# Performance work log

Measured on AMD Instinct MI355X. Metric: run time of the kernel, lower is better.

## Reference

```python
import jax, jax.numpy as jnp
import numpy as np

VOCAB = 32000      # embedding vocab
EMBED = 300        # nn.Embedding embedding_dim
HID = 256          # sequence_size // 2 per direction (sequence_size=512)
N_COLS = 4096      # number of columns (split-delimited segments)
SEG_LEN = 8        # 7 description words + 1 SPLIT token per column
SPLIT_IDX = 0
T = N_COLS * SEG_LEN


def setup_inputs() -> dict:
    key = jax.random.key(0)
    ks = jax.random.split(key, 10)
    # tokens in [1, VOCAB), with SPLIT_IDX at the end of every SEG_LEN block
    seq = jax.random.randint(ks[0], (T,), 1, VOCAB)
    seq = seq.at[SEG_LEN - 1::SEG_LEN].set(SPLIT_IDX)
    s = 1.0 / np.sqrt(HID)  # torch LSTM default init range

    def u(k, shape):
        return jax.random.uniform(k, shape, jnp.float32, -s, s)

    return {
        "emb_table": jax.random.normal(ks[1], (VOCAB, EMBED), jnp.float32),
        "w_ih_f": u(ks[2], (4 * HID, EMBED)),
        "w_hh_f": u(ks[3], (4 * HID, HID)),
        "b_ih_f": u(ks[4], (4 * HID,)),
        "b_hh_f": u(ks[5], (4 * HID,)),
        "w_ih_b": u(ks[6], (4 * HID, EMBED)),
        "w_hh_b": u(ks[7], (4 * HID, HID)),
        "b_ih_b": u(ks[8], (4 * HID,)),
        "b_hh_b": u(ks[9], (4 * HID,)),
        "seq_s": seq,
    }


def _run_dir(xg, mask, w_hh, reverse):
    """Masked LSTM over time. xg: [L, N, 4H] precomputed input gates (+bias),
    mask: [L, N] validity per original time index. Returns final hidden [N, H]."""
    if reverse:
        xg = xg[::-1]
        mask = mask[::-1]
    N = xg.shape[1]

    def step(carry, inp):
        h, c = carry
        g, m = inp
        gates = g + h @ w_hh.T                       # [N, 4H]
        i, f, gg, o = jnp.split(gates, 4, axis=-1)   # torch gate order i,f,g,o
        c_new = jax.nn.sigmoid(f) * c + jax.nn.sigmoid(i) * jnp.tanh(gg)
        h_new = jax.nn.sigmoid(o) * jnp.tanh(c_new)
        m = m[:, None]
        return (jnp.where(m, h_new, h), jnp.where(m, c_new, c)), None

    init = (jnp.zeros((N, HID), xg.dtype), jnp.zeros((N, HID), xg.dtype))
    (h, _), _ = jax.lax.scan(step, init, (xg, mask))
    return h


def reference(emb_table, w_ih_f, w_hh_f, b_ih_f, b_hh_f,
              w_ih_b, w_hh_b, b_ih_b, b_hh_b, seq_s):
    col = jnp.arange(N_COLS)
    # torch code: ends = nonzero(split); begins = roll(ends,1); begins[0] = 0
    # => segment i>0 starts AT the previous split token (len SEG_LEN);
    #    segment 0 is [0, SEG_LEN-1) (len SEG_LEN-1).
    begins = jnp.where(col == 0, 0, col * SEG_LEN - 1)
    lengths = jnp.where(col == 0, SEG_LEN - 1, SEG_LEN)
    idx = jnp.clip(begins[:, None] + jnp.arange(SEG_LEN)[None, :], 0, T - 1)  # [N, L]
    mask = jnp.arange(SEG_LEN)[None, :] < lengths[:, None]                    # [N, L]

    segs = emb_table[seq_s][idx]        # [N, L, E] embedded ragged segments
    x = segs.transpose(1, 0, 2)          # [L, N, E]
    m = mask.T                           # [L, N]

    xg_f = jnp.einsum('lne,ge->lng', x, w_ih_f) + b_ih_f + b_hh_f
    xg_b = jnp.einsum('lne,ge->lng', x, w_ih_b) + b_ih_b + b_hh_b
    h_f = _run_dir(xg_f, m, w_hh_f, reverse=False)   # forward final hidden
    h_b = _run_dir(xg_b, m, w_hh_b, reverse=True)    # backward final hidden (t=0)
    # torch final_hidden.view(-1) per column == concat(fwd, bwd)
    return jnp.concatenate([h_f, h_b], axis=-1)      # [N_COLS, 2*HID]
```

## Files before the change

### kernel.cpp

```cpp
#include <hip/hip_runtime.h>

typedef unsigned int uint;
typedef unsigned short ushort;
typedef __attribute__((ext_vector_type(8))) short short8;
typedef __attribute__((ext_vector_type(4))) float f32x4;
typedef __attribute__((ext_vector_type(4))) uint uint4w;

#define T_LEN 32768
#define EMB 300
#define HID 256
#define NCOLS 4096

__device__ __forceinline__ ushort f2bf(float f) {
  uint u = __float_as_uint(f);
  return (ushort)((u + 0x7fffu + ((u >> 16) & 1u)) >> 16);
}
__device__ __forceinline__ float bf2f(ushort u) {
  return __uint_as_float(((uint)u) << 16);
}
__device__ __forceinline__ float sigm(float x) { return 1.f / (1.f + __expf(-x)); }
__device__ __forceinline__ float tanh_(float x) { return 2.f / (1.f + __expf(-2.f * x)) - 1.f; }

__device__ __forceinline__ void gload_lds16(const void* g, void* l) {
  __builtin_amdgcn_global_load_lds((const __attribute__((address_space(1))) void*)g,
                                   (__attribute__((address_space(3))) void*)l, 16, 0, 0);
}

__global__ void prep_kernel(const float* __restrict__ emb,
                            const float* __restrict__ wihf, const float* __restrict__ whhf,
                            const float* __restrict__ bihf, const float* __restrict__ bhhf,
                            const float* __restrict__ wihb, const float* __restrict__ whhb,
                            const float* __restrict__ bihb, const float* __restrict__ bhhb,
                            const int* __restrict__ seq,
                            ushort* __restrict__ X, ushort* __restrict__ Wih,
                            ushort* __restrict__ Whh, float* __restrict__ bias) {
  const int NX = T_LEN * 40;
  const int NWIH = 2048 * 40;
  const int NWHH = 2048 * 32;
  const int NB = 2048;
  const int total = NX + NWIH + NWHH + NB;
  for (int t = blockIdx.x * blockDim.x + threadIdx.x; t < total; t += gridDim.x * blockDim.x) {
    if (t < NX) {
      int r = t / 40, k8 = t % 40, k = k8 * 8;
      int col = r >> 3, j = r & 7;
      int tok = (col == 0) ? j : (col * 8 - 1 + j);
      const float* src = emb + (long)seq[tok] * EMB + k;
      alignas(16) ushort tmp[8];
#pragma unroll
      for (int i = 0; i < 8; ++i) tmp[i] = (k + i < EMB) ? f2bf(src[i]) : (ushort)0;
      *(uint4w*)(X + (long)r * 320 + k) = *(const uint4w*)tmp;
    } else if (t < NX + NWIH) {
      int t2 = t - NX;
      int n = t2 / 40, k8 = t2 % 40, k = k8 * 8;
      const float* src = ((n < 1024) ? wihf : wihb) + (long)(n & 1023) * EMB + k;
      alignas(16) ushort tmp[8];
#pragma unroll
      for (int i = 0; i < 8; ++i) tmp[i] = (k + i < EMB) ? f2bf(src[i]) : (ushort)0;
      *(uint4w*)(Wih + (long)n * 320 + k) = *(const uint4w*)tmp;
    } else if (t < NX + NWIH + NWHH) {
      int t3 = t - NX - NWIH;
      int n = t3 / 32, k8 = t3 % 32, k = k8 * 8;
      const float* src = ((n < 1024) ? whhf : whhb) + (long)(n & 1023) * HID + k;
      alignas(16) ushort tmp[8];
#pragma unroll
      for (int i = 0; i < 8; ++i) tmp[i] = f2bf(src[i]);
      *(uint4w*)(Whh + (long)n * 256 + k) = *(const uint4w*)tmp;
    } else {
      int n = t - NX - NWIH - NWHH;
      bias[n] = (n < 1024) ? (bihf[n] + bhhf[n]) : (bihb[n - 1024] + bhhb[n - 1024]);
    }
  }
}

__global__ void gemm_xg_kernel(const ushort* __restrict__ X, const ushort* __restrict__ Wih,
                               const float* __restrict__ bias, ushort* __restrict__ xg) {
  __shared__ ushort a_lds[2][128 * 32];
  const int tid = threadIdx.x;
  const int lane = tid & 63, w = tid >> 6;
  const int wr = w >> 1, wc = w & 1;
  const int qrow = lane >> 4, ln = lane & 15;
  const int m0 = blockIdx.x * 128, n0 = blockIdx.y * 128;

  auto stage = [&](int buf, int kt) {
#pragma unroll
    for (int q = 0; q < 2; ++q) {
      int byteoff = w * 2048 + q * 1024 + lane * 16;
      int row = byteoff >> 6, koff = byteoff & 63;
      const char* src = (const char*)X + (long)(m0 + row) * 640 + kt * 64 + koff;
      void* dst = (char*)&a_lds[buf][0] + w * 2048 + q * 1024;
      gload_lds16(src, dst);
    }
  };

  const ushort* wb = Wih + (long)(n0 + wc * 64 + ln) * 320 + qrow * 8;
  auto loadB = [&](short8 (&dst)[4], int kt) {
#pragma unroll
    for (int nt = 0; nt < 4; ++nt)
      dst[nt] = *(const short8*)(wb + nt * 16 * 320 + kt * 32);
  };

  const f32x4 fzero = {0.f, 0.f, 0.f, 0.f};
  f32x4 acc[4][4];
#pragma unroll
  for (int i = 0; i < 4; ++i)
#pragma unroll
    for (int jj = 0; jj < 4; ++jj) acc[i][jj] = fzero;

  auto gemmK = [&](short8 (&b)[4], int buf) {
    short8 a[4];
#pragma unroll
    for (int rt = 0; rt < 4; ++rt)
      a[rt] = *(const short8*)&a_lds[buf][(wr * 64 + rt * 16 + ln) * 32 + qrow * 8];
#pragma unroll
    for (int rt = 0; rt < 4; ++rt)
#pragma unroll
      for (int nt = 0; nt < 4; ++nt)
        acc[rt][nt] = __builtin_amdgcn_mfma_f32_16x16x32_bf16(a[rt], b[nt], acc[rt][nt], 0, 0, 0);
  };

  short8 bA[4], bB[4];
  stage(0, 0);
  loadB(bA, 0);
#pragma unroll 1
  for (int kt2 = 0; kt2 < 5; ++kt2) {
    const int kt = kt2 * 2;
    __syncthreads();
    loadB(bB, kt + 1);
    __builtin_amdgcn_sched_barrier(0);
    if (kt < 9) stage(1, kt + 1);
    __builtin_amdgcn_sched_barrier(0);
    gemmK(bA, 0);
    __syncthreads();
    if (kt2 < 4) loadB(bA, kt + 2);
    __builtin_amdgcn_sched_barrier(0);
    if (kt + 2 < 10) stage(0, kt + 2);
    __builtin_amdgcn_sched_barrier(0);
    gemmK(bB, 1);
  }

  ushort* sbuf = &a_lds[0][0];
  float bv[4];
#pragma unroll
  for (int nt = 0; nt < 4; ++nt) bv[nt] = bias[n0 + wc * 64 + nt * 16 + ln];
#pragma unroll
  for (int R = 0; R < 4; ++R) {
    __syncthreads();
#pragma unroll
    for (int nt = 0; nt < 4; ++nt)
#pragma unroll
      for (int r = 0; r < 4; ++r)
        sbuf[(wr * 16 + qrow * 4 + r) * 128 + wc * 64 + nt * 16 + ln] = f2bf(acc[R][nt][r] + bv[nt]);
    __syncthreads();
#pragma unroll
    for (int p = 0; p < 2; ++p) {
      int row = p * 16 + (tid >> 4);
      int c0 = (tid & 15) * 8;
      uint4w v = *(uint4w*)&sbuf[row * 128 + c0];
      *(uint4w*)&xg[(long)(m0 + (row >> 4) * 64 + R * 16 + (row & 15)) * 2048 + n0 + c0] = v;
    }
  }
}

__global__ __launch_bounds__(512, 2) void lstm_kernel(const ushort* __restrict__ xg,
                                                      const ushort* __restrict__ Whh,
                                                      float* __restrict__ out) {
  __shared__ ushort h_lds[32][264];
  __shared__ ushort xg_lds[2][32][1024];
  const int tid = threadIdx.x;
  const int lane = tid & 63, w = tid >> 6;
  const int qrow = lane >> 4, ln = lane & 15;
  const int bid = blockIdx.x;
  const int d = bid >> 7, cg = bid & 127;

  const ushort* wbase = Whh + (long)(d * 1024 + w * 32 + ln) * 256 + qrow * 8;

  float c_st[2][2][4], h_st[2][2][4];
#pragma unroll
  for (int rt = 0; rt < 2; ++rt)
#pragma unroll
    for (int q = 0; q < 2; ++q)
#pragma unroll
      for (int r = 0; r < 4; ++r) { c_st[rt][q][r] = 0.f; h_st[rt][q][r] = 0.f; }

  auto stage = [&](int buf, int j) {
#pragma unroll
    for (int q = 0; q < 8; ++q) {
      int byteoff = w * 8192 + q * 1024 + lane * 16;
      int cloc = byteoff >> 11, noff = byteoff & 2047;
      const char* src = (const char*)xg + (long)((cg * 32 + cloc) * 8 + j) * 4096 + d * 2048 + noff;
      void* dst = (char*)&xg_lds[0][0][0] + buf * 65536 + w * 8192 + q * 1024;
      gload_lds16(src, dst);
    }
  };

  const f32x4 fzero = {0.f, 0.f, 0.f, 0.f};

  stage(0, d ? 7 : 0);

#pragma unroll 1
  for (int it = 0; it < 8; ++it) {
    __syncthreads();
    const int buf = it & 1;

    f32x4 acc[4][2][2];
#pragma unroll
    for (int g = 0; g < 4; ++g)
#pragma unroll
      for (int q = 0; q < 2; ++q)
#pragma unroll
        for (int rt = 0; rt < 2; ++rt) acc[g][q][rt] = fzero;

    if (it > 0) {
      auto loadB = [&](short8 (&dst)[4][2], int ks) {
#pragma unroll
        for (int g = 0; g < 4; ++g)
#pragma unroll
          for (int q = 0; q < 2; ++q)
            dst[g][q] = *(const short8*)(wbase + g * 65536 + q * 4096 + ks * 32);
      };
      auto gemmK = [&](short8 (&b)[4][2], int ks) {
        short8 a0 = *(const short8*)&h_lds[ln][ks * 32 + qrow * 8];
        short8 a1 = *(const short8*)&h_lds[16 + ln][ks * 32 + qrow * 8];
#pragma unroll
        for (int g = 0; g < 4; ++g)
#pragma unroll
          for (int q = 0; q < 2; ++q) {
            acc[g][q][0] = __builtin_amdgcn_mfma_f32_16x16x32_bf16(a0, b[g][q], acc[g][q][0], 0, 0, 0);
            acc[g][q][1] = __builtin_amdgcn_mfma_f32_16x16x32_bf16(a1, b[g][q], acc[g][q][1], 0, 0, 0);
          }
      };
      short8 bA[4][2], bB[4][2];
      loadB(bA, 0);
      loadB(bB, 1);
      gemmK(bA, 0); loadB(bA, 2);
      gemmK(bB, 1); loadB(bB, 3);
      gemmK(bA, 2); loadB(bA, 4);
      gemmK(bB, 3); loadB(bB, 5);
      gemmK(bA, 4); loadB(bA, 6);
      gemmK(bB, 5); loadB(bB, 7);
      gemmK(bA, 6);
      gemmK(bB, 7);
    }

    __builtin_amdgcn_sched_barrier(0);
    if (it < 7) stage((it + 1) & 1, d ? (6 - it) : (it + 1));
    __builtin_amdgcn_sched_barrier(0);

    asm volatile("s_waitcnt lgkmcnt(0)" ::: "memory");
    __builtin_amdgcn_s_barrier();

    const bool mstep = d ? (it == 0) : (it == 7);
#pragma unroll
    for (int rt = 0; rt < 2; ++rt)
#pragma unroll
      for (int q = 0; q < 2; ++q)
#pragma unroll
        for (int r = 0; r < 4; ++r) {
          int cc = rt * 16 + qrow * 4 + r;
          int hid = w * 32 + q * 16 + ln;
          float pi = acc[0][q][rt][r] + bf2f(xg_lds[buf][cc][hid]);
          float pf = acc[1][q][rt][r] + bf2f(xg_lds[buf][cc][256 + hid]);
          float pg = acc[2][q][rt][r] + bf2f(xg_lds[buf][cc][512 + hid]);
          float po = acc[3][q][rt][r] + bf2f(xg_lds[buf][cc][768 + hid]);
          float cn = sigm(pf) * c_st[rt][q][r] + sigm(pi) * tanh_(pg);
          float hn = sigm(po) * tanh_(cn);
          bool skip = mstep && (cg == 0) && (cc == 0);
          if (!skip) { c_st[rt][q][r] = cn; h_st[rt][q][r] = hn; }
          h_lds[cc][hid] = f2bf(h_st[rt][q][r]);
        }
  }

#pragma unroll
  for (int rt = 0; rt < 2; ++rt)
#pragma unroll
    for (int q = 0; q < 2; ++q)
#pragma unroll
      for (int r = 0; r < 4; ++r) {
        int cc = rt * 16 + qrow * 4 + r;
        int hid = w * 32 + q * 16 + ln;
        out[(long)(cg * 32 + cc) * 512 + d * 256 + hid] = h_st[rt][q][r];
      }
}

extern "C" void kernel_launch(void* const* d_in, const int* in_sizes, int n_in,
                              void* d_out, int out_size, void* d_ws, size_t ws_size,
                              hipStream_t stream) {
  const float* emb  = (const float*)d_in[0];
  const float* wihf = (const float*)d_in[1];
  const float* whhf = (const float*)d_in[2];
  const float* bihf = (const float*)d_in[3];
  const float* bhhf = (const float*)d_in[4];
  const float* wihb = (const float*)d_in[5];
  const float* whhb = (const float*)d_in[6];
  const float* bihb = (const float*)d_in[7];
  const float* bhhb = (const float*)d_in[8];
  const int*   seq  = (const int*)d_in[9];
  float* out = (float*)d_out;

  char* ws = (char*)d_ws;
  ushort* xg   = (ushort*)(ws);
  ushort* X    = (ushort*)(ws + 134217728);
  ushort* Wih  = (ushort*)(ws + 155189248);
  ushort* Whh  = (ushort*)(ws + 156499968);
  float*  bias = (float*)(ws + 157548544);

  prep_kernel<<<dim3(1024), dim3(256), 0, stream>>>(emb, wihf, whhf, bihf, bhhf,
                                                    wihb, whhb, bihb, bhhb, seq,
                                                    X, Wih, Whh, bias);
  gemm_xg_kernel<<<dim3(256, 16), dim3(256), 0, stream>>>(X, Wih, bias, xg);
  lstm_kernel<<<dim3(256), dim3(512), 0, stream>>>(xg, Whh, out);
}
```

Measured before the change: 276.4 us.

## Stream pre-swizzled Whh through triple-buffered LDS and load xg gates into registers

The prep kernel now writes the recurrent weights in a swizzled layout grouped by k-slice and gate pair. In the LSTM kernel, each slice is pulled into a three-deep LDS ring with async global-to-LDS loads, using vmcnt waits and barriers, instead of each wave loading B fragments straight from global memory. The xg staging buffer in LDS is removed; each thread gathers its gate pre-activations from global memory into registers just before the cell update. The aim is to hide weight-fetch latency behind the MFMA work, at the cost of more barriers per step and many scattered 2-byte xg loads.

```diff
diff --git a/kernel.cpp b/kernel.cpp
--- a/kernel.cpp
+++ b/kernel.cpp
@@ -33,7 +33,7 @@
                             const float* __restrict__ bihb, const float* __restrict__ bhhb,
                             const int* __restrict__ seq,
                             ushort* __restrict__ X, ushort* __restrict__ Wih,
-                            ushort* __restrict__ Whh, float* __restrict__ bias) {
+                            ushort* __restrict__ Whh2, float* __restrict__ bias) {
   const int NX = T_LEN * 40;
   const int NWIH = 2048 * 40;
   const int NWHH = 2048 * 32;
@@ -59,12 +59,15 @@
       *(uint4w*)(Wih + (long)n * 320 + k) = *(const uint4w*)tmp;
     } else if (t < NX + NWIH + NWHH) {
       int t3 = t - NX - NWIH;
-      int n = t3 / 32, k8 = t3 % 32, k = k8 * 8;
-      const float* src = ((n < 1024) ? whhf : whhb) + (long)(n & 1023) * HID + k;
+      int n = t3 / 32, k8 = t3 % 32;
+      int dd = n >> 10, rowg = n & 1023;
+      int gp = rowg >> 9, rr = rowg & 511;
+      int s = (k8 >> 2) * 2 + gp, c = k8 & 3;
+      const float* src = ((dd == 0) ? whhf : whhb) + (long)rowg * HID + k8 * 8;
       alignas(16) ushort tmp[8];
 #pragma unroll
       for (int i = 0; i < 8; ++i) tmp[i] = f2bf(src[i]);
-      *(uint4w*)(Whh + (long)n * 256 + k) = *(const uint4w*)tmp;
+      *(uint4w*)(Whh2 + ((((long)dd * 16 + s) * 4 + c) * 512 + rr) * 8) = *(const uint4w*)tmp;
     } else {
       int n = t - NX - NWIH - NWHH;
       bias[n] = (n < 1024) ? (bihf[n] + bhhf[n]) : (bihb[n - 1024] + bhhb[n - 1024]);
@@ -161,18 +164,18 @@
   }
 }
 
-__global__ __launch_bounds__(512, 2) void lstm_kernel(const ushort* __restrict__ xg,
-                                                      const ushort* __restrict__ Whh,
-                                                      float* __restrict__ out) {
+__global__ __launch_bounds__(512) void lstm_kernel(const ushort* __restrict__ xg,
+                                                   const ushort* __restrict__ Whh2,
+                                                   float* __restrict__ out) {
   __shared__ ushort h_lds[32][264];
-  __shared__ ushort xg_lds[2][32][1024];
+  __shared__ alignas(16) char b_lds[3][32768];
   const int tid = threadIdx.x;
   const int lane = tid & 63, w = tid >> 6;
   const int qrow = lane >> 4, ln = lane & 15;
   const int bid = blockIdx.x;
   const int d = bid >> 7, cg = bid & 127;
 
-  const ushort* wbase = Whh + (long)(d * 1024 + w * 32 + ln) * 256 + qrow * 8;
+  for (int i = tid; i < 32 * 264 / 2; i += 512) ((uint*)h_lds)[i] = 0u;
 
   float c_st[2][2][4], h_st[2][2][4];
 #pragma unroll
@@ -182,25 +185,19 @@
 #pragma unroll
       for (int r = 0; r < 4; ++r) { c_st[rt][q][r] = 0.f; h_st[rt][q][r] = 0.f; }
 
-  auto stage = [&](int buf, int j) {
-#pragma unroll
-    for (int q = 0; q < 8; ++q) {
-      int byteoff = w * 8192 + q * 1024 + lane * 16;
-      int cloc = byteoff >> 11, noff = byteoff & 2047;
-      const char* src = (const char*)xg + (long)((cg * 32 + cloc) * 8 + j) * 4096 + d * 2048 + noff;
-      void* dst = (char*)&xg_lds[0][0][0] + buf * 65536 + w * 8192 + q * 1024;
-      gload_lds16(src, dst);
-    }
+  auto stageB = [&](int s, int bufi) {
+    const char* src = (const char*)Whh2 + (((long)(d * 16 + s)) << 15) + w * 4096 + lane * 16;
+    char* dst = &b_lds[bufi][0] + w * 4096;
+#pragma unroll
+    for (int q2 = 0; q2 < 4; ++q2) gload_lds16(src + q2 * 1024, dst + q2 * 1024);
   };
 
   const f32x4 fzero = {0.f, 0.f, 0.f, 0.f};
-
-  stage(0, d ? 7 : 0);
 
 #pragma unroll 1
   for (int it = 0; it < 8; ++it) {
-    __syncthreads();
-    const int buf = it & 1;
+    const int j = d ? (7 - it) : it;
+    __syncthreads();
 
     f32x4 acc[4][2][2];
 #pragma unroll
@@ -211,43 +208,47 @@
         for (int rt = 0; rt < 2; ++rt) acc[g][q][rt] = fzero;
 
     if (it > 0) {
-      auto loadB = [&](short8 (&dst)[4][2], int ks) {
-#pragma unroll
-        for (int g = 0; g < 4; ++g)
-#pragma unroll
-          for (int q = 0; q < 2; ++q)
-            dst[g][q] = *(const short8*)(wbase + g * 65536 + q * 4096 + ks * 32);
-      };
-      auto gemmK = [&](short8 (&b)[4][2], int ks) {
+#pragma unroll
+      for (int ks = 0; ks < 8; ++ks) {
         short8 a0 = *(const short8*)&h_lds[ln][ks * 32 + qrow * 8];
         short8 a1 = *(const short8*)&h_lds[16 + ln][ks * 32 + qrow * 8];
 #pragma unroll
-        for (int g = 0; g < 4; ++g)
-#pragma unroll
-          for (int q = 0; q < 2; ++q) {
-            acc[g][q][0] = __builtin_amdgcn_mfma_f32_16x16x32_bf16(a0, b[g][q], acc[g][q][0], 0, 0, 0);
-            acc[g][q][1] = __builtin_amdgcn_mfma_f32_16x16x32_bf16(a1, b[g][q], acc[g][q][1], 0, 0, 0);
-          }
-      };
-      short8 bA[4][2], bB[4][2];
-      loadB(bA, 0);
-      loadB(bB, 1);
-      gemmK(bA, 0); loadB(bA, 2);
-      gemmK(bB, 1); loadB(bB, 3);
-      gemmK(bA, 2); loadB(bA, 4);
-      gemmK(bB, 3); loadB(bB, 5);
-      gemmK(bA, 4); loadB(bA, 6);
-      gemmK(bB, 5); loadB(bB, 7);
-      gemmK(bA, 6);
-      gemmK(bB, 7);
+        for (int gp = 0; gp < 2; ++gp) {
+          const int s = ks * 2 + gp;
+          if (s == 15) { asm volatile("s_waitcnt vmcnt(0)" ::: "memory"); }
+          else         { asm volatile("s_waitcnt vmcnt(4)" ::: "memory"); }
+          __builtin_amdgcn_s_barrier();
+          asm volatile("" ::: "memory");
+          if (s <= 13) stageB(s + 2, (s + 2) % 3);
+          const char* bb = &b_lds[s % 3][0];
+#pragma unroll
+          for (int gi = 0; gi < 2; ++gi)
+#pragma unroll
+            for (int q = 0; q < 2; ++q) {
+              short8 b = *(const short8*)(bb + qrow * 8192 + (gi * 256 + w * 32 + q * 16 + ln) * 16);
+              const int g = gp * 2 + gi;
+              acc[g][q][0] = __builtin_amdgcn_mfma_f32_16x16x32_bf16(a0, b, acc[g][q][0], 0, 0, 0);
+              acc[g][q][1] = __builtin_amdgcn_mfma_f32_16x16x32_bf16(a1, b, acc[g][q][1], 0, 0, 0);
+            }
+        }
+      }
     }
 
-    __builtin_amdgcn_sched_barrier(0);
-    if (it < 7) stage((it + 1) & 1, d ? (6 - it) : (it + 1));
-    __builtin_amdgcn_sched_barrier(0);
+    const ushort* xgb = xg + (long)(cg * 256 + j) * 2048 + qrow * 65536 + d * 1024 + w * 32 + ln;
+    ushort xv[2][2][4][4];
+#pragma unroll
+    for (int rt = 0; rt < 2; ++rt)
+#pragma unroll
+      for (int q = 0; q < 2; ++q)
+#pragma unroll
+        for (int r = 0; r < 4; ++r)
+#pragma unroll
+          for (int g = 0; g < 4; ++g)
+            xv[rt][q][r][g] = xgb[(long)rt * 262144 + r * 16384 + g * 256 + q * 16];
 
     asm volatile("s_waitcnt lgkmcnt(0)" ::: "memory");
     __builtin_amdgcn_s_barrier();
+    asm volatile("" ::: "memory");
 
     const bool mstep = d ? (it == 0) : (it == 7);
 #pragma unroll
@@ -258,16 +259,18 @@
         for (int r = 0; r < 4; ++r) {
           int cc = rt * 16 + qrow * 4 + r;
           int hid = w * 32 + q * 16 + ln;
-          float pi = acc[0][q][rt][r] + bf2f(xg_lds[buf][cc][hid]);
-          float pf = acc[1][q][rt][r] + bf2f(xg_lds[buf][cc][256 + hid]);
-          float pg = acc[2][q][rt][r] + bf2f(xg_lds[buf][cc][512 + hid]);
-          float po = acc[3][q][rt][r] + bf2f(xg_lds[buf][cc][768 + hid]);
+          float pi = acc[0][q][rt][r] + bf2f(xv[rt][q][r][0]);
+          float pf = acc[1][q][rt][r] + bf2f(xv[rt][q][r][1]);
+          float pg = acc[2][q][rt][r] + bf2f(xv[rt][q][r][2]);
+          float po = acc[3][q][rt][r] + bf2f(xv[rt][q][r][3]);
           float cn = sigm(pf) * c_st[rt][q][r] + sigm(pi) * tanh_(pg);
           float hn = sigm(po) * tanh_(cn);
           bool skip = mstep && (cg == 0) && (cc == 0);
           if (!skip) { c_st[rt][q][r] = cn; h_st[rt][q][r] = hn; }
           h_lds[cc][hid] = f2bf(h_st[rt][q][r]);
         }
+
+    if (it < 7) { stageB(0, 0); stageB(1, 1); }
   }
 
 #pragma unroll
@@ -301,12 +304,12 @@
   ushort* xg   = (ushort*)(ws);
   ushort* X    = (ushort*)(ws + 134217728);
   ushort* Wih  = (ushort*)(ws + 155189248);
-  ushort* Whh  = (ushort*)(ws + 156499968);
+  ushort* Whh2 = (ushort*)(ws + 156499968);
   float*  bias = (float*)(ws + 157548544);
 
   prep_kernel<<<dim3(1024), dim3(256), 0, stream>>>(emb, wihf, whhf, bihf, bhhf,
                                                     wihb, whhb, bihb, bhhb, seq,
-                                                    X, Wih, Whh, bias);
+                                                    X, Wih, Whh2, bias);
   gemm_xg_kernel<<<dim3(256, 16), dim3(256), 0, stream>>>(X, Wih, bias, xg);
-  lstm_kernel<<<dim3(256), dim3(512), 0, stream>>>(xg, Whh, out);
-}
+  lstm_kernel<<<dim3(256), dim3(512), 0, stream>>>(xg, Whh2, out);
+}
```

Result: no change. 271.8 us (-1.7%).
